# Kernel tuning notes

Hardware: AMD Instinct MI355X
Metric: run time of the kernel (lower is better)

Reference implementation:

```python
import jax, jax.numpy as jnp
import numpy as np

D_MODEL = 2048
NUM_HEADS = 16
HEAD_DIM = D_MODEL // NUM_HEADS
LAYER_IDX = 0
NUM_LAYERS = 13
REINIT_LAMBDA = 0.8


def setup_inputs() -> dict:
    key = jax.random.key(0)
    ks = jax.random.split(key, 8)
    B, S = 2, 2048
    x = jax.random.normal(ks[0], (B, S, D_MODEL), dtype=jnp.float32)
    init = 1.0 / np.sqrt(D_MODEL)
    def w(k):
        return jax.random.uniform(k, (D_MODEL, D_MODEL), dtype=jnp.float32, minval=-init, maxval=init)
    lam_init = REINIT_LAMBDA * ((LAYER_IDX + 1) / NUM_LAYERS)
    return {
        "x": x,
        "q1_w": w(ks[1]), "k1_w": w(ks[2]),
        "q2_w": w(ks[3]), "k2_w": w(ks[4]),
        "v_w": w(ks[5]), "o_w": w(ks[6]),
        "lambda_param": jnp.full((NUM_HEADS,), lam_init, dtype=jnp.float32),
    }


def _heads(t, B, S):
    # [B, S, D] -> [B, H, S, Dh]
    return t.reshape(B, S, NUM_HEADS, HEAD_DIM).transpose(0, 2, 1, 3)


def reference(x, q1_w, k1_w, q2_w, k2_w, v_w, o_w, lambda_param):
    B, S, _ = x.shape
    # nn.Linear(bias=False): y = x @ W.T, W is [out, in]
    q1 = _heads(x @ q1_w.T, B, S)
    k1 = _heads(x @ k1_w.T, B, S)
    q2 = _heads(x @ q2_w.T, B, S)
    k2 = _heads(x @ k2_w.T, B, S)
    v = _heads(x @ v_w.T, B, S)
    scale = jnp.sqrt(jnp.float32(HEAD_DIM))
    attn1 = jax.nn.softmax(jnp.einsum('bhqd,bhkd->bhqk', q1, k1) / scale, axis=-1)
    attn2 = jax.nn.softmax(jnp.einsum('bhqd,bhkd->bhqk', q2, k2) / scale, axis=-1)
    lam = lambda_param.reshape(1, NUM_HEADS, 1, 1)
    out = jnp.einsum('bhqk,bhkd->bhqd', attn1 - lam * attn2, v)
    out = out.transpose(0, 2, 1, 3).reshape(B, S, D_MODEL)
    return out @ o_w.T
```

## Files before the change

### kernel.cpp

```cpp
#include <hip/hip_runtime.h>
#include <hip/hip_bf16.h>
#include <stdint.h>

typedef __bf16 bf16_t;
typedef __bf16 bf16x8 __attribute__((ext_vector_type(8)));
typedef float f32x4 __attribute__((ext_vector_type(4)));

#define D_MODEL 2048
#define SEQ     2048
#define NHEADS  16
#define HDIM    128
#define BATCH   2
#define NTOK    (BATCH * SEQ)
#define NELEM   ((size_t)BATCH * SEQ * D_MODEL)
#define D2      ((size_t)D_MODEL * D_MODEL)

__global__ void __launch_bounds__(256)
cvt7_kernel(const float* __restrict__ x,
            const float* __restrict__ w0, const float* __restrict__ w1,
            const float* __restrict__ w2, const float* __restrict__ w3,
            const float* __restrict__ w4, const float* __restrict__ w5,
            bf16_t* __restrict__ xb, bf16_t* __restrict__ wb) {
  const int y = blockIdx.y;
  const float* srcs[7] = {x, w0, w1, w2, w3, w4, w5};
  const float* src = srcs[y];
  bf16_t* dst = (y == 0) ? xb : wb + (size_t)(y - 1) * D2;
  const size_t n = (y == 0) ? NELEM : D2;
  const size_t base = ((size_t)blockIdx.x * 256 + threadIdx.x) * 8;
  if (base >= n) return;
  f32x4 lo = *(const f32x4*)(src + base);
  f32x4 hi = *(const f32x4*)(src + base + 4);
  union { bf16x8 v; bf16_t h[8]; } u;
#pragma unroll
  for (int j = 0; j < 4; j++) {
    u.h[j]     = (bf16_t)lo[j];
    u.h[j + 4] = (bf16_t)hi[j];
  }
  *(bf16x8*)(dst + base) = u.v;
}

__device__ __forceinline__ void async_load16(const void* g, void* l) {
  __builtin_amdgcn_global_load_lds(
      (const __attribute__((address_space(1))) void*)g,
      (__attribute__((address_space(3))) void*)l, 16, 0, 0);
}

template <int TRANS, typename TC>
__device__ __forceinline__ void gemm_tile_body(const bf16_t* __restrict__ A,
                                               const bf16_t* __restrict__ W,
                                               TC* __restrict__ C) {
  extern __shared__ char smem[];
  bf16_t* As = (bf16_t*)smem;
  bf16_t* Bs = (bf16_t*)smem + 128 * 32;
  const int K = D_MODEL, N = D_MODEL;
  const int tid  = threadIdx.x;
  const int wave = tid >> 6, lane = tid & 63;
  const int quad = lane >> 4, l16 = lane & 15;
  const int tm = blockIdx.x * 128, tn = blockIdx.y * 128;
  const int wm = (wave & 1) * 64, wn = (wave >> 1) * 64;

  f32x4 acc[4][4];
#pragma unroll
  for (int i = 0; i < 4; i++)
#pragma unroll
    for (int j = 0; j < 4; j++) acc[i][j] = (f32x4){0.f, 0.f, 0.f, 0.f};

  const int srow = lane >> 2;
  const int scol = (lane & 3) * 8;

  for (int k0 = 0; k0 < K; k0 += 32) {
    __syncthreads();
#pragma unroll
    for (int i = 0; i < 2; i++) {
      const int rbase = (i * 4 + wave) * 16;
      async_load16(A + (size_t)(tm + rbase + srow) * K + k0 + scol, As + rbase * 32);
      async_load16(W + (size_t)(tn + rbase + srow) * K + k0 + scol, Bs + rbase * 32);
    }
    __syncthreads();

    bf16x8 af[4], bfr[4];
#pragma unroll
    for (int i = 0; i < 4; i++)
      af[i] = *(const bf16x8*)(As + (wm + i * 16 + l16) * 32 + quad * 8);
#pragma unroll
    for (int j = 0; j < 4; j++)
      bfr[j] = *(const bf16x8*)(Bs + (wn + j * 16 + l16) * 32 + quad * 8);
#pragma unroll
    for (int i = 0; i < 4; i++)
#pragma unroll
      for (int j = 0; j < 4; j++)
        acc[i][j] = __builtin_amdgcn_mfma_f32_16x16x32_bf16(af[i], bfr[j], acc[i][j], 0, 0, 0);
  }

#pragma unroll
  for (int i = 0; i < 4; i++) {
    const int r0 = wm + i * 16 + quad * 4;
#pragma unroll
    for (int j = 0; j < 4; j++) {
      const int c = tn + wn + j * 16 + l16;
      if constexpr (TRANS) {
        const int m = tm + r0;
        const int b = m >> 11;
        const int s = m & (SEQ - 1);
        union { bf16_t h[4]; uint2 u2; } p;
#pragma unroll
        for (int r = 0; r < 4; r++) p.h[r] = (bf16_t)acc[i][j][r];
        *(uint2*)((bf16_t*)C + (size_t)(b * D_MODEL + c) * SEQ + s) = p.u2;
      } else {
#pragma unroll
        for (int r = 0; r < 4; r++)
          C[(size_t)(tm + r0 + r) * N + c] = (TC)acc[i][j][r];
      }
    }
  }
}

__global__ void __launch_bounds__(256)
gemm_out_kernel(const bf16_t* __restrict__ A, const bf16_t* __restrict__ W,
                float* __restrict__ C) {
  gemm_tile_body<0, float>(A, W, C);
}

__global__ void __launch_bounds__(256)
gemm_vt_kernel(const bf16_t* __restrict__ A, const bf16_t* __restrict__ W,
               bf16_t* __restrict__ C) {
  gemm_tile_body<1, bf16_t>(A, W, C);
}

template <int TRANS, typename TC>
__device__ __forceinline__ void gemm256_body(const bf16_t* __restrict__ A,
                                             const bf16_t* __restrict__ W,
                                             TC* __restrict__ C,
                                             const int tm, const int tn) {
  extern __shared__ char smem[];
  constexpr int K = D_MODEL;
  constexpr int NT = K / 64;
  const int tid = threadIdx.x;
  const int wid = tid >> 6, lane = tid & 63;
  const int quad = lane >> 4, l16 = lane & 15;
  const int wm = wid >> 2, wn = wid & 3;

  const int sr = lane >> 2;
  const int sc = (lane & 3) ^ ((lane >> 4) & 2);
  const int rdoff = (l16 * 64 + quad * 16) ^ ((l16 & 8) << 2);

  f32x4 acc[8][4];
#pragma unroll
  for (int i = 0; i < 8; i++)
#pragma unroll
    for (int j = 0; j < 4; j++) acc[i][j] = (f32x4){0.f, 0.f, 0.f, 0.f};

  bf16x8 af[2][4], bfA[2][2], bfB[2][2];

#define STAGE256(P, rowbase, ldsbase, h, t)                                      \
  {                                                                              \
    const bf16_t* _s = (P) + (size_t)((rowbase) + (h) * 128 + wid * 16 + sr) * K \
                           + ((t) * 64 + sc * 8);                                \
    char* _d = smem + (ldsbase) + (h) * 16384 + wid * 2048;                      \
    async_load16(_s, _d);                                                        \
    async_load16(_s + 32, _d + 1024);                                            \
  }

#define LDA256(c, rh)                                                            \
  _Pragma("unroll") for (int ks = 0; ks < 2; ks++)                               \
  _Pragma("unroll") for (int j = 0; j < 4; j++)                                  \
      af[ks][j] = *(const bf16x8*)(smem + (c) * 65536 +                          \
                  ((wm * 8 + (rh) * 4 + j) * 2 + ks) * 1024 + rdoff);

#define LDB256(c, dst, cf0)                                                      \
  _Pragma("unroll") for (int ks = 0; ks < 2; ks++)                               \
  _Pragma("unroll") for (int j = 0; j < 2; j++)                                  \
      dst[ks][j] = *(const bf16x8*)(smem + (c) * 65536 + 32768 +                 \
                   ((wn * 4 + (cf0) + j) * 2 + ks) * 1024 + rdoff);

#define MFMA16(rh, bfr, cb)                                                      \
  _Pragma("unroll") for (int j = 0; j < 4; j++)                                  \
  _Pragma("unroll") for (int cf = 0; cf < 2; cf++)                               \
  _Pragma("unroll") for (int ks = 0; ks < 2; ks++)                               \
      acc[(rh) * 4 + j][(cb) + cf] = __builtin_amdgcn_mfma_f32_16x16x32_bf16(    \
          af[ks][j], bfr[ks][cf], acc[(rh) * 4 + j][(cb) + cf], 0, 0, 0);

#define BAR256() __builtin_amdgcn_s_barrier()
#define LGKM0()                                                                  \
  { asm volatile("s_waitcnt lgkmcnt(0)" ::: "memory");                           \
    __builtin_amdgcn_sched_barrier(0); }
#define VMW4()                                                                   \
  { asm volatile("s_waitcnt vmcnt(4)" ::: "memory");                             \
    __builtin_amdgcn_sched_barrier(0); }
#define VMW0()                                                                   \
  { asm volatile("s_waitcnt vmcnt(0)" ::: "memory");                             \
    __builtin_amdgcn_sched_barrier(0); }

  STAGE256(A, tm, 0,     0, 0); STAGE256(A, tm, 0,     1, 0);
  STAGE256(W, tn, 32768, 0, 0); STAGE256(W, tn, 32768, 1, 0);
  STAGE256(W, tn, 98304, 0, 1); STAGE256(W, tn, 98304, 1, 1);
  VMW4();
  BAR256();

  for (int it = 0; it < NT / 2; ++it) {
    const int kt = 2 * it;
    const int t2 = (kt + 2 < NT) ? kt + 2 : 0;
    const int t3 = (kt + 3 < NT) ? kt + 3 : 0;

    LDA256(0, 0); LDB256(0, bfA, 0);
    STAGE256(A, tm, 65536, 0, kt + 1);
    BAR256(); LGKM0();
    __builtin_amdgcn_s_setprio(1); MFMA16(0, bfA, 0); __builtin_amdgcn_s_setprio(0);
    BAR256();
    LDB256(0, bfB, 2);
    STAGE256(A, tm, 65536, 1, kt + 1);
    BAR256(); LGKM0();
    __builtin_amdgcn_s_setprio(1); MFMA16(0, bfB, 2); __builtin_amdgcn_s_setprio(0);
    BAR256();
    LDA256(0, 1);
    STAGE256(W, tn, 32768, 0, t2);
    BAR256(); LGKM0();
    __builtin_amdgcn_s_setprio(1); MFMA16(1, bfA, 0); __builtin_amdgcn_s_setprio(0);
    BAR256();
    STAGE256(W, tn, 32768, 1, t2);
    BAR256();
    __builtin_amdgcn_s_setprio(1); MFMA16(1, bfB, 2); __builtin_amdgcn_s_setprio(0);
    VMW4();
    BAR256();
    LDA256(1, 0); LDB256(1, bfA, 0);
    STAGE256(A, tm, 0, 0, t2);
    BAR256(); LGKM0();
    __builtin_amdgcn_s_setprio(1); MFMA16(0, bfA, 0); __builtin_amdgcn_s_setprio(0);
    BAR256();
    LDB256(1, bfB, 2);
    STAGE256(A, tm, 0, 1, t2);
    BAR256(); LGKM0();
    __builtin_amdgcn_s_setprio(1); MFMA16(0, bfB, 2); __builtin_amdgcn_s_setprio(0);
    BAR256();
    LDA256(1, 1);
    STAGE256(W, tn, 98304, 0, t3);
    BAR256(); LGKM0();
    __builtin_amdgcn_s_setprio(1); MFMA16(1, bfA, 0); __builtin_amdgcn_s_setprio(0);
    BAR256();
    STAGE256(W, tn, 98304, 1, t3);
    BAR256();
    __builtin_amdgcn_s_setprio(1); MFMA16(1, bfB, 2); __builtin_amdgcn_s_setprio(0);
    VMW4();
    BAR256();
  }
  VMW0();

#pragma unroll
  for (int rf = 0; rf < 8; rf++) {
    const int r0 = wm * 128 + rf * 16 + quad * 4;
#pragma unroll
    for (int cf = 0; cf < 4; cf++) {
      const int c = tn + wn * 64 + cf * 16 + l16;
      if constexpr (TRANS) {
        const int m = tm + r0;
        const int b = m >> 11;
        const int s = m & (SEQ - 1);
        union { bf16_t h[4]; uint2 u2; } p;
#pragma unroll
        for (int r = 0; r < 4; r++) p.h[r] = (bf16_t)acc[rf][cf][r];
        *(uint2*)((bf16_t*)C + (size_t)(b * D_MODEL + c) * SEQ + s) = p.u2;
      } else {
#pragma unroll
        for (int r = 0; r < 4; r++)
          C[(size_t)(tm + r0 + r) * D_MODEL + c] = (TC)acc[rf][cf][r];
      }
    }
  }
#undef STAGE256
#undef LDA256
#undef LDB256
#undef MFMA16
#undef BAR256
#undef LGKM0
#undef VMW4
#undef VMW0
}

__global__ void __launch_bounds__(512, 2)
proj4_kernel(const bf16_t* __restrict__ xb, const bf16_t* __restrict__ wb,
             bf16_t* __restrict__ q1, bf16_t* __restrict__ k1,
             bf16_t* __restrict__ q2, bf16_t* __restrict__ k2) {
  const int g = blockIdx.y;
  const int orig = blockIdx.x;
  const int wg = (orig & 7) * 16 + (orig >> 3);
  const int tm = (wg & 15) * 256;
  const int tn = (wg >> 4) * 256;
  const bf16_t* w = wb + (size_t)g * D2;
  bf16_t* o = (g == 0) ? q1 : (g == 1) ? k1 : (g == 2) ? q2 : k2;
  gemm256_body<0, bf16_t>(xb, w, o, tm, tn);
}

__global__ void __launch_bounds__(256, 2)
diff_attn_kernel(const bf16_t* __restrict__ q1g, const bf16_t* __restrict__ k1g,
                 const bf16_t* __restrict__ q2g, const bf16_t* __restrict__ k2g,
                 const bf16_t* __restrict__ vtg, const float* __restrict__ lamg,
                 bf16_t* __restrict__ outg) {
  const int blk = blockIdx.x;
  const int xcd = blk & 7;
  const int idx = blk >> 3;
  const int bh  = xcd * 4 + (idx >> 5);
  const int qt  = idx & 31;
  const int b = bh >> 4, h = bh & 15;
  const int tid = threadIdx.x, wave = tid >> 6, lane = tid & 63;
  const int quad = lane >> 4, l16 = lane & 15;
  const int stream = wave >> 1;
  const int wq     = wave & 1;
  const int q0 = qt * 64 + wq * 32;

  __shared__ char smem_all[81920];
  bf16_t* K1b = (bf16_t*)smem_all;
  bf16_t* K2b = (bf16_t*)(smem_all + 32768);
  bf16_t* Vs  = (bf16_t*)(smem_all + 65536);

  const bf16_t* k1p = k1g + (size_t)b * SEQ * D_MODEL + h * HDIM;
  const bf16_t* k2p = k2g + (size_t)b * SEQ * D_MODEL + h * HDIM;
  const bf16_t* vtp = vtg + ((size_t)b * D_MODEL + h * HDIM) * SEQ;
  const bf16_t* qp  = (stream ? q2g : q1g) +
                      ((size_t)b * SEQ + q0) * D_MODEL + h * HDIM;
  const bf16_t* Ksb = stream ? K2b : K1b;

  bf16x8 aqa[4], aqb[4];
#pragma unroll
  for (int c = 0; c < 4; c++) {
    aqa[c] = *(const bf16x8*)(qp + (size_t)l16 * D_MODEL + c * 32 + quad * 8);
    aqb[c] = *(const bf16x8*)(qp + (size_t)(16 + l16) * D_MODEL + c * 32 + quad * 8);
  }

  f32x4 Oa[8], Ob[8];
#pragma unroll
  for (int n = 0; n < 8; n++) {
    Oa[n] = (f32x4){0.f, 0.f, 0.f, 0.f};
    Ob[n] = (f32x4){0.f, 0.f, 0.f, 0.f};
  }
  float la = 0.f, lb = 0.f;

  const float c2 = 0.0883883476483184f * 1.4426950408889634f;

  const int k_r  = lane >> 4;
  const int k_p  = lane & 15;
  const int v_r  = lane >> 3;
  const int v_p  = lane & 7;

#define STAGE_K(KT, BUF)                                                         \
  { _Pragma("unroll") for (int i = 0; i < 4; i++) {                              \
      const int krb = wave * 16 + i * 4;                                         \
      const int kr  = krb + k_r;                                                 \
      const int kkey = (((kr >> 2) & 3) << 3) | (((kr >> 4) & 1) << 2) |         \
                       (kr & 3) | (kr & 32);                                     \
      const int kg = k_p ^ (kr & 7);                                             \
      async_load16(k1p + (size_t)((KT) + kkey) * D_MODEL + kg * 8,               \
                   K1b + (BUF) * 8192 + krb * 128);                              \
      async_load16(k2p + (size_t)((KT) + kkey) * D_MODEL + kg * 8,               \
                   K2b + (BUF) * 8192 + krb * 128);                              \
  } }

#define STAGE_V(KT)                                                              \
  { _Pragma("unroll") for (int i = 0; i < 4; i++) {                              \
      const int vrb = wave * 32 + i * 8;                                         \
      const int vr  = vrb + v_r;                                                 \
      const int vg  = v_p ^ (vr & 7);                                            \
      async_load16(vtp + (size_t)vr * SEQ + (KT) + vg * 8, Vs + vrb * 64);       \
  } }

#define VMW(N)                                                                   \
  { asm volatile("s_waitcnt vmcnt(" #N ")" ::: "memory");                        \
    __builtin_amdgcn_sched_barrier(0); }
#define BARR()                                                                   \
  { __builtin_amdgcn_s_barrier();                                                \
    __builtin_amdgcn_sched_barrier(0); }

  STAGE_K(0, 0);
  STAGE_V(0);
  VMW(0); BARR();

  for (int t = 0; t < SEQ / 64; ++t) {
    const int ktn = (t < SEQ / 64 - 1) ? (t + 1) * 64 : 0;
    STAGE_K(ktn, (t + 1) & 1);
    VMW(12);
    BARR();

    const bf16_t* Kc = Ksb + (t & 1) * 8192;
    const int xsw = l16 & 7;

    f32x4 sa[4], sb[4];
#pragma unroll
    for (int s = 0; s < 4; s++) {
      sa[s] = (f32x4){0.f, 0.f, 0.f, 0.f};
      sb[s] = (f32x4){0.f, 0.f, 0.f, 0.f};
    }
    __builtin_amdgcn_s_setprio(1);
#pragma unroll
    for (int c = 0; c < 4; c++) {
      const int pos = ((c * 4 + quad) ^ xsw) * 8;
#pragma unroll
      for (int s = 0; s < 4; s++) {
        bf16x8 f = *(const bf16x8*)(Kc + (s * 16 + l16) * 128 + pos);
        sa[s] = __builtin_amdgcn_mfma_f32_16x16x32_bf16(f, aqa[c], sa[s], 0, 0, 0);
        sb[s] = __builtin_amdgcn_mfma_f32_16x16x32_bf16(f, aqb[c], sb[s], 0, 0, 0);
      }
    }
    __builtin_amdgcn_s_setprio(0);

    union { bf16x8 v; bf16_t h[8]; } pa[2], pb[2];
#pragma unroll
    for (int s = 0; s < 4; s++) {
#pragma unroll
      for (int r = 0; r < 4; r++) {
        const float ea = __builtin_amdgcn_exp2f(sa[s][r] * c2);
        const float eb = __builtin_amdgcn_exp2f(sb[s][r] * c2);
        pa[s >> 1].h[(s & 1) * 4 + r] = (bf16_t)ea; la += ea;
        pb[s >> 1].h[(s & 1) * 4 + r] = (bf16_t)eb; lb += eb;
      }
    }

    VMW(8);
    BARR();

    __builtin_amdgcn_s_setprio(1);
#pragma unroll
    for (int half = 0; half < 2; half++) {
      const int vpos = ((half * 4 + quad) ^ xsw) * 8;
#pragma unroll
      for (int n = 0; n < 8; n++) {
        bf16x8 vf = *(const bf16x8*)(Vs + (n * 16 + l16) * 64 + vpos);
        Oa[n] = __builtin_amdgcn_mfma_f32_16x16x32_bf16(pa[half].v, vf, Oa[n], 0, 0, 0);
        Ob[n] = __builtin_amdgcn_mfma_f32_16x16x32_bf16(pb[half].v, vf, Ob[n], 0, 0, 0);
      }
    }
    __builtin_amdgcn_s_setprio(0);

    BARR();
    STAGE_V(ktn);
  }
#undef STAGE_K
#undef STAGE_V
#undef VMW
#undef BARR

  la += __shfl_xor(la, 16); la += __shfl_xor(la, 32);
  lb += __shfl_xor(lb, 16); lb += __shfl_xor(lb, 32);

  __syncthreads();
  float* xfer = (float*)smem_all;

  if (stream == 1) {
    const float lam = lamg[h];
    const float ia = lam / la, ib = lam / lb;
    float iao[4], ibo[4];
#pragma unroll
    for (int r = 0; r < 4; r++) {
      iao[r] = __shfl(ia, quad * 4 + r, 16);
      ibo[r] = __shfl(ib, quad * 4 + r, 16);
    }
#pragma unroll
    for (int r = 0; r < 4; r++)
#pragma unroll
      for (int n = 0; n < 8; n++) {
        xfer[(wq * 32 + quad * 4 + r) * 128 + n * 16 + l16] = Oa[n][r] * iao[r];
        xfer[(wq * 32 + 16 + quad * 4 + r) * 128 + n * 16 + l16] = Ob[n][r] * ibo[r];
      }
  }
  __syncthreads();
  if (stream == 0) {
    const float ia = 1.f / la, ib = 1.f / lb;
    float iao[4], ibo[4];
#pragma unroll
    for (int r = 0; r < 4; r++) {
      iao[r] = __shfl(ia, quad * 4 + r, 16);
      ibo[r] = __shfl(ib, quad * 4 + r, 16);
    }
    bf16_t* op = outg + ((size_t)b * SEQ + q0) * D_MODEL + h * HDIM;
#pragma unroll
    for (int r = 0; r < 4; r++)
#pragma unroll
      for (int n = 0; n < 8; n++) {
        const float va = Oa[n][r] * iao[r] -
                         xfer[(wq * 32 + quad * 4 + r) * 128 + n * 16 + l16];
        const float vb = Ob[n][r] * ibo[r] -
                         xfer[(wq * 32 + 16 + quad * 4 + r) * 128 + n * 16 + l16];
        op[(size_t)(quad * 4 + r) * D_MODEL + n * 16 + l16] = (bf16_t)va;
        op[(size_t)(16 + quad * 4 + r) * D_MODEL + n * 16 + l16] = (bf16_t)vb;
      }
  }
}

extern "C" void kernel_launch(void* const* d_in, const int* in_sizes, int n_in,
                              void* d_out, int out_size, void* d_ws, size_t ws_size,
                              hipStream_t stream) {
  const float* x   = (const float*)d_in[0];
  const float* wq1 = (const float*)d_in[1];
  const float* wk1 = (const float*)d_in[2];
  const float* wq2 = (const float*)d_in[3];
  const float* wk2 = (const float*)d_in[4];
  const float* wv  = (const float*)d_in[5];
  const float* wo  = (const float*)d_in[6];
  const float* lam = (const float*)d_in[7];

  bf16_t* ws = (bf16_t*)d_ws;
  bf16_t* q1 = ws + 0 * NELEM;
  bf16_t* k1 = ws + 1 * NELEM;
  bf16_t* q2 = ws + 2 * NELEM;
  bf16_t* k2 = ws + 3 * NELEM;
  bf16_t* vt = ws + 4 * NELEM;
  bf16_t* xb = ws + 5 * NELEM;
  bf16_t* ao = xb;
  bf16_t* wb = ws + 6 * NELEM;

  static bool attr_set = false;
  if (!attr_set) {
    (void)hipFuncSetAttribute(reinterpret_cast<const void*>(proj4_kernel),
                              hipFuncAttributeMaxDynamicSharedMemorySize, 131072);
    attr_set = true;
  }

  cvt7_kernel<<<dim3(4096, 7), dim3(256), 0, stream>>>(
      x, wq1, wk1, wq2, wk2, wv, wo, xb, wb);
  proj4_kernel<<<dim3(128, 4), dim3(512), 131072, stream>>>(
      xb, wb, q1, k1, q2, k2);
  gemm_vt_kernel<<<dim3(NTOK / 128, D_MODEL / 128), dim3(256), 16384, stream>>>(
      xb, wb + 4 * D2, vt);
  diff_attn_kernel<<<dim3(BATCH * NHEADS * (SEQ / 64)), dim3(256), 0, stream>>>(
      q1, k1, q2, k2, vt, lam, ao);
  gemm_out_kernel<<<dim3(NTOK / 128, D_MODEL / 128), dim3(256), 16384, stream>>>(
      ao, wb + 5 * D2, (float*)d_out);
}
```

Before: 515.7 us.

## Single-buffer K in diff attention for 3 blocks/CU and fold softmax scale into weights

Drops the K double buffer so shared memory per block shrinks from 80KB to 48KB, and raises launch bounds to allow three resident blocks per CU. The K prefetch for the next tile now starts after the QK MFMAs, with an extra barrier and wait at the end of each iteration. Separately, the softmax scale times log2(e) is multiplied into the q1 and q2 weights during the bf16 conversion, which removes one multiply per score. The cost is less overlap of K loads with compute, another barrier per iteration, and tighter register limits. Pre-scaling in bf16 also changes rounding slightly.

```diff
diff --git a/kernel.cpp b/kernel.cpp
--- a/kernel.cpp
+++ b/kernel.cpp
@@ -26,6 +26,8 @@
   const float* src = srcs[y];
   bf16_t* dst = (y == 0) ? xb : wb + (size_t)(y - 1) * D2;
   const size_t n = (y == 0) ? NELEM : D2;
+  const float scl = (y == 1 || y == 3)
+      ? (0.0883883476483184f * 1.4426950408889634f) : 1.0f;
   const size_t base = ((size_t)blockIdx.x * 256 + threadIdx.x) * 8;
   if (base >= n) return;
   f32x4 lo = *(const f32x4*)(src + base);
@@ -33,8 +35,8 @@
   union { bf16x8 v; bf16_t h[8]; } u;
 #pragma unroll
   for (int j = 0; j < 4; j++) {
-    u.h[j]     = (bf16_t)lo[j];
-    u.h[j + 4] = (bf16_t)hi[j];
+    u.h[j]     = (bf16_t)(lo[j] * scl);
+    u.h[j + 4] = (bf16_t)(hi[j] * scl);
   }
   *(bf16x8*)(dst + base) = u.v;
 }
@@ -290,7 +292,7 @@
   gemm256_body<0, bf16_t>(xb, w, o, tm, tn);
 }
 
-__global__ void __launch_bounds__(256, 2)
+__global__ void __launch_bounds__(256, 3)
 diff_attn_kernel(const bf16_t* __restrict__ q1g, const bf16_t* __restrict__ k1g,
                  const bf16_t* __restrict__ q2g, const bf16_t* __restrict__ k2g,
                  const bf16_t* __restrict__ vtg, const float* __restrict__ lamg,
@@ -307,17 +309,17 @@
   const int wq     = wave & 1;
   const int q0 = qt * 64 + wq * 32;
 
-  __shared__ char smem_all[81920];
-  bf16_t* K1b = (bf16_t*)smem_all;
-  bf16_t* K2b = (bf16_t*)(smem_all + 32768);
-  bf16_t* Vs  = (bf16_t*)(smem_all + 65536);
+  __shared__ char smem_all[49152];
+  bf16_t* K1s = (bf16_t*)smem_all;
+  bf16_t* K2s = (bf16_t*)(smem_all + 16384);
+  bf16_t* Vs  = (bf16_t*)(smem_all + 32768);
 
   const bf16_t* k1p = k1g + (size_t)b * SEQ * D_MODEL + h * HDIM;
   const bf16_t* k2p = k2g + (size_t)b * SEQ * D_MODEL + h * HDIM;
   const bf16_t* vtp = vtg + ((size_t)b * D_MODEL + h * HDIM) * SEQ;
   const bf16_t* qp  = (stream ? q2g : q1g) +
                       ((size_t)b * SEQ + q0) * D_MODEL + h * HDIM;
-  const bf16_t* Ksb = stream ? K2b : K1b;
+  const bf16_t* Ksp = stream ? K2s : K1s;
 
   bf16x8 aqa[4], aqb[4];
 #pragma unroll
@@ -333,15 +335,13 @@
     Ob[n] = (f32x4){0.f, 0.f, 0.f, 0.f};
   }
   float la = 0.f, lb = 0.f;
-
-  const float c2 = 0.0883883476483184f * 1.4426950408889634f;
 
   const int k_r  = lane >> 4;
   const int k_p  = lane & 15;
   const int v_r  = lane >> 3;
   const int v_p  = lane & 7;
 
-#define STAGE_K(KT, BUF)                                                         \
+#define STAGE_K(KT)                                                              \
   { _Pragma("unroll") for (int i = 0; i < 4; i++) {                              \
       const int krb = wave * 16 + i * 4;                                         \
       const int kr  = krb + k_r;                                                 \
@@ -349,9 +349,9 @@
                        (kr & 3) | (kr & 32);                                     \
       const int kg = k_p ^ (kr & 7);                                             \
       async_load16(k1p + (size_t)((KT) + kkey) * D_MODEL + kg * 8,               \
-                   K1b + (BUF) * 8192 + krb * 128);                              \
+                   K1s + krb * 128);                                             \
       async_load16(k2p + (size_t)((KT) + kkey) * D_MODEL + kg * 8,               \
-                   K2b + (BUF) * 8192 + krb * 128);                              \
+                   K2s + krb * 128);                                             \
   } }
 
 #define STAGE_V(KT)                                                              \
@@ -369,17 +369,12 @@
   { __builtin_amdgcn_s_barrier();                                                \
     __builtin_amdgcn_sched_barrier(0); }
 
-  STAGE_K(0, 0);
+  STAGE_K(0);
   STAGE_V(0);
-  VMW(0); BARR();
+  VMW(4); BARR();
 
   for (int t = 0; t < SEQ / 64; ++t) {
     const int ktn = (t < SEQ / 64 - 1) ? (t + 1) * 64 : 0;
-    STAGE_K(ktn, (t + 1) & 1);
-    VMW(12);
-    BARR();
-
-    const bf16_t* Kc = Ksb + (t & 1) * 8192;
     const int xsw = l16 & 7;
 
     f32x4 sa[4], sb[4];
@@ -394,20 +389,23 @@
       const int pos = ((c * 4 + quad) ^ xsw) * 8;
 #pragma unroll
       for (int s = 0; s < 4; s++) {
-        bf16x8 f = *(const bf16x8*)(Kc + (s * 16 + l16) * 128 + pos);
+        bf16x8 f = *(const bf16x8*)(Ksp + (s * 16 + l16) * 128 + pos);
         sa[s] = __builtin_amdgcn_mfma_f32_16x16x32_bf16(f, aqa[c], sa[s], 0, 0, 0);
         sb[s] = __builtin_amdgcn_mfma_f32_16x16x32_bf16(f, aqb[c], sb[s], 0, 0, 0);
       }
     }
     __builtin_amdgcn_s_setprio(0);
 
+    BARR();
+    STAGE_K(ktn);
+
     union { bf16x8 v; bf16_t h[8]; } pa[2], pb[2];
 #pragma unroll
     for (int s = 0; s < 4; s++) {
 #pragma unroll
       for (int r = 0; r < 4; r++) {
-        const float ea = __builtin_amdgcn_exp2f(sa[s][r] * c2);
-        const float eb = __builtin_amdgcn_exp2f(sb[s][r] * c2);
+        const float ea = __builtin_amdgcn_exp2f(sa[s][r]);
+        const float eb = __builtin_amdgcn_exp2f(sb[s][r]);
         pa[s >> 1].h[(s & 1) * 4 + r] = (bf16_t)ea; la += ea;
         pb[s >> 1].h[(s & 1) * 4 + r] = (bf16_t)eb; lb += eb;
       }
@@ -431,6 +429,8 @@
 
     BARR();
     STAGE_V(ktn);
+    VMW(4);
+    BARR();
   }
 #undef STAGE_K
 #undef STAGE_V
```

Result: slower. 881.1 us (+70.9%).
